# Optimization experiments

Hardware: AMD Instinct MI355X
Metric: run time of the kernel (lower is better)

## Reference

```python
import jax, jax.numpy as jnp
import numpy as np

B, S, H, D = 2, 2048, 16, 64


def setup_inputs() -> dict:
    key = jax.random.key(0)
    kq, kk, kv, km = jax.random.split(key, 4)
    q = jax.random.normal(kq, (B, S, H, D), dtype=jnp.float32)
    k = jax.random.normal(kk, (B, S, H, D), dtype=jnp.float32)
    v = jax.random.normal(kv, (B, S, H, D), dtype=jnp.float32)
    key_padding_mask = jax.random.randint(km, (B, S), 0, 2).astype(bool)
    return {"q": q, "k": k, "v": v, "key_padding_mask": key_padding_mask}


def reference(q, k, v, key_padding_mask):
    # [B,S,H,D] -> [B,H,S,D]; fp32 upcast (inputs already fp32)
    qt = jnp.transpose(q, (0, 2, 1, 3)).astype(jnp.float32)
    kt = jnp.transpose(k, (0, 2, 1, 3)).astype(jnp.float32)
    vt = jnp.transpose(v, (0, 2, 1, 3)).astype(jnp.float32)
    scale = D ** (-0.5)
    # [B,H,Sq,Sk]
    scores = jnp.einsum("bhqd,bhkd->bhqk", qt, kt) * scale
    # masked_fill where key_padding_mask is True -> -inf
    mask = key_padding_mask[:, None, None, :]  # [B,1,1,Sk]
    scores = jnp.where(mask, -jnp.inf, scores)
    attn = jax.nn.softmax(scores, axis=-1)
    out = jnp.einsum("bhqk,bhkd->bhqd", attn, vt).astype(q.dtype)
    # back to [B,S,H,D]
    return jnp.transpose(out, (0, 2, 1, 3))
```

## Files before the change

### kernel.cpp

```cpp
#include <hip/hip_runtime.h>
#include <hip/hip_bf16.h>

#define BB 2
#define SS 2048
#define HH 16
#define DD 64
#define BR 128
#define BC 64
#define NT (SS / BC)
#define NQT (SS / BR)
#define TILE_E (BC * DD)
#define TILE_B (TILE_E * 2)
#define LOG2E 1.44269504f
#define LSTR 72
#define OSZ (BB * SS * HH * DD)

typedef __attribute__((ext_vector_type(8))) short short8;
typedef __attribute__((ext_vector_type(4))) float f32x4;
typedef __attribute__((ext_vector_type(16))) float f32x16;
typedef __attribute__((ext_vector_type(4))) unsigned int uint32x4;
typedef __attribute__((ext_vector_type(4))) unsigned short ushort4_t;

static __device__ __forceinline__ unsigned short f2bf(float f) {
    unsigned int u = __float_as_uint(f);
    unsigned int r = u + 0x7FFFu + ((u >> 16) & 1u);
    return (unsigned short)(r >> 16);
}
static __device__ __forceinline__ unsigned int cvtpk(float lo, float hi) {
    unsigned int r;
    asm("v_cvt_pk_bf16_f32 %0, %1, %2" : "=v"(r) : "v"(lo), "v"(hi));
    return r;
}
static __device__ __forceinline__ void pl32swap(unsigned int &a, unsigned int &b) {
#if __has_builtin(__builtin_amdgcn_permlane32_swap)
    const auto r = __builtin_amdgcn_permlane32_swap((int)a, (int)b, false, false);
    a = (unsigned int)r[0];
    b = (unsigned int)r[1];
#else
    asm("v_permlane32_swap_b32 %0, %1" : "+v"(a), "+v"(b));
#endif
}
static __device__ __forceinline__ float fexp2(float x) {
#if __has_builtin(__builtin_amdgcn_exp2f)
    return __builtin_amdgcn_exp2f(x);
#else
    return exp2f(x);
#endif
}
static __device__ __forceinline__ void gl_lds16(const void* g, void* l) {
    __builtin_amdgcn_global_load_lds(
        (const __attribute__((address_space(1))) void*)g,
        (__attribute__((address_space(3))) void*)l, 16, 0, 0);
}

__global__ __launch_bounds__(256, 2)
void prep_kernel(const float* __restrict__ K, const float* __restrict__ V,
                 const int* __restrict__ M,
                 unsigned short* __restrict__ Kb, unsigned short* __restrict__ Vt,
                 int* __restrict__ mcnt)
{
    __shared__ unsigned short Vl[DD * LSTR];

    const int t  = blockIdx.x & (NT - 1);
    const int b  = blockIdx.x >> 9;
    const int bh = blockIdx.x >> 5;
    const int tid = threadIdx.x;
    const size_t tile = (size_t)blockIdx.x * TILE_E;
    const size_t rs = (size_t)HH * DD;
    const float* kb0 = K + (((size_t)b * SS + t * BC) * HH + (bh & 15)) * DD;
    const float* vb0 = V + (((size_t)b * SS + t * BC) * HH + (bh & 15)) * DD;
    const int* mrow = M + (size_t)b * SS + t * BC;

    {
        const int p  = tid & 7;
        const int r0 = tid >> 3;
        #pragma unroll
        for (int half = 0; half < 2; ++half) {
            const int r = r0 + half * 32;
            const int c = p ^ (r & 7);
            const float sel = mrow[r] ? 0.0f : 1.0f;
            const float* ks = kb0 + (size_t)r * rs + c * 8;
            const float4 f0 = *(const float4*)ks;
            const float4 f1 = *(const float4*)(ks + 4);
            uint32x4 u;
            u[0] = cvtpk(f0.x * sel, f0.y * sel);
            u[1] = cvtpk(f0.z * sel, f0.w * sel);
            u[2] = cvtpk(f1.x * sel, f1.y * sel);
            u[3] = cvtpk(f1.z * sel, f1.w * sel);
            *(uint32x4*)(Kb + tile + r * 64 + p * 8) = u;
        }
    }
    {
        const int vr = tid >> 2;
        const int vc = tid & 3;
        const float sel = mrow[vr] ? 0.0f : 1.0f;
        const float* vp = vb0 + (size_t)vr * rs + vc * 16;
        #pragma unroll
        for (int i = 0; i < 4; ++i) {
            const float4 f = *(const float4*)(vp + i * 4);
            const int d = vc * 16 + i * 4;
            Vl[(d + 0) * LSTR + vr] = f2bf(f.x * sel);
            Vl[(d + 1) * LSTR + vr] = f2bf(f.y * sel);
            Vl[(d + 2) * LSTR + vr] = f2bf(f.z * sel);
            Vl[(d + 3) * LSTR + vr] = f2bf(f.w * sel);
        }
    }
    __syncthreads();
    {
        const int p  = tid & 7;
        const int r0 = tid >> 3;
        #pragma unroll
        for (int half = 0; half < 2; ++half) {
            const int r = r0 + half * 32;
            const int c = p ^ (r & 7);
            const short8 o = *(const short8*)&Vl[r * LSTR + c * 8];
            *(short8*)(Vt + tile + r * 64 + p * 8) = o;
        }
    }
    if ((bh & 15) == 0 && tid < 64) {
        const unsigned long long bal = __ballot(mrow[tid] != 0);
        if (tid == 0) mcnt[b * NT + t] = (int)__popcll(bal);
    }
}

template<bool SPLIT>
__global__ __launch_bounds__(256, 2)
void fa3_kernel(const float* __restrict__ Q,
                const unsigned short* __restrict__ Kb,
                const unsigned short* __restrict__ Vt,
                const int* __restrict__ mcnt,
                float* __restrict__ Op,
                float* __restrict__ Lp)
{
    __shared__ __align__(16) unsigned short Ks[2][2 * TILE_E];
    __shared__ __align__(16) unsigned short Vs[2][2 * TILE_E];

    const int nwg  = (SPLIT ? 2 * BB * HH * NQT : BB * HH * NQT);
    const int cpx  = nwg >> 3;
    const int blk  = (blockIdx.x & 7) * cpx + (blockIdx.x >> 3);

    const int qt  = blk & (NQT - 1);
    const int bh  = (blk >> 4) & 31;
    const int spl = SPLIT ? (blk >> 9) : 0;
    const int b   = bh >> 4;
    const int h   = bh & 15;
    const int kt0 = SPLIT ? spl * (NT / 2) : 0;
    const int ktn = SPLIT ? (NT / 2) : NT;

    const int tid  = threadIdx.x;
    const int wave = tid >> 6;
    const int lane = tid & 63;
    const int ln   = lane & 31;
    const int l5   = lane >> 5;

    const float qscale = 0.125f * LOG2E;
    const int qrow = qt * BR + wave * 32 + ln;
    const float* qp = Q + (((size_t)b * SS + qrow) * HH + h) * DD;
    short8 qf[4];
    #pragma unroll
    for (int t = 0; t < 4; ++t) {
        const int d0 = t * 16 + l5 * 8;
        const float4 f0 = *(const float4*)(qp + d0);
        const float4 f1 = *(const float4*)(qp + d0 + 4);
        uint32x4 u;
        u[0] = cvtpk(f0.x * qscale, f0.y * qscale);
        u[1] = cvtpk(f0.z * qscale, f0.w * qscale);
        u[2] = cvtpk(f1.x * qscale, f1.y * qscale);
        u[3] = cvtpk(f1.z * qscale, f1.w * qscale);
        qf[t] = __builtin_bit_cast(short8, u);
    }

    int corr = 0;
    for (int i = 0; i < ktn; ++i) corr += mcnt[b * NT + kt0 + i];

    f32x16 acc0, acc1;
    #pragma unroll
    for (int i = 0; i < 16; ++i) { acc0[i] = 0.f; acc1[i] = 0.f; }
    f32x4 lsum4 = {0.f, 0.f, 0.f, 0.f};

    const unsigned short* kb_bh = Kb + (size_t)bh * NT * TILE_E;
    const unsigned short* vt_bh = Vt + (size_t)bh * NT * TILE_E;
    const int we = wave * 1024;
    const int wb = wave * 2048;

    {
        const unsigned short* kbt = kb_bh + (size_t)kt0 * TILE_E;
        const unsigned short* vtt = vt_bh + (size_t)kt0 * TILE_E;
        #pragma unroll
        for (int s = 0; s < 2; ++s) {
            gl_lds16(kbt + s * TILE_E + we + lane * 8,       (char*)Ks[0] + s * TILE_B + wb);
            gl_lds16(kbt + s * TILE_E + we + 512 + lane * 8, (char*)Ks[0] + s * TILE_B + wb + 1024);
            gl_lds16(vtt + s * TILE_E + we + lane * 8,       (char*)Vs[0] + s * TILE_B + wb);
            gl_lds16(vtt + s * TILE_E + we + 512 + lane * 8, (char*)Vs[0] + s * TILE_B + wb + 1024);
        }
    }
    __syncthreads();

    const int pswz = (ln & 7);
    const int npair = ktn >> 1;

    for (int ii = 0; ii < npair; ++ii) {
        const int cur = ii & 1;
        const int nxt = cur ^ 1;
        const int kn = kt0 + 2 * ((ii + 1 < npair) ? ii + 1 : ii);
        const unsigned short* kbt = kb_bh + (size_t)kn * TILE_E;
        const unsigned short* vtt = vt_bh + (size_t)kn * TILE_E;
        #pragma unroll
        for (int s = 0; s < 2; ++s) {
            gl_lds16(kbt + s * TILE_E + we + lane * 8,       (char*)Ks[nxt] + s * TILE_B + wb);
            gl_lds16(kbt + s * TILE_E + we + 512 + lane * 8, (char*)Ks[nxt] + s * TILE_B + wb + 1024);
            gl_lds16(vtt + s * TILE_E + we + lane * 8,       (char*)Vs[nxt] + s * TILE_B + wb);
            gl_lds16(vtt + s * TILE_E + we + 512 + lane * 8, (char*)Vs[nxt] + s * TILE_B + wb + 1024);
        }

        #pragma unroll
        for (int sub = 0; sub < 2; ++sub) {
            const unsigned short* Kt = Ks[cur] + sub * TILE_E;
            const unsigned short* Vtl = Vs[cur] + sub * TILE_E;

            f32x16 s0, s1;
            #pragma unroll
            for (int i = 0; i < 16; ++i) { s0[i] = 0.f; s1[i] = 0.f; }
            #pragma unroll
            for (int t = 0; t < 4; ++t) {
                const int p = (2 * t + l5) ^ pswz;
                const short8 kf0 = *(const short8*)(Kt + ln * 64 + p * 8);
                const short8 kf1 = *(const short8*)(Kt + (32 + ln) * 64 + p * 8);
                s0 = __builtin_amdgcn_mfma_f32_32x32x16_bf16(kf0, qf[t], s0, 0, 0, 0);
                s1 = __builtin_amdgcn_mfma_f32_32x32x16_bf16(kf1, qf[t], s1, 0, 0, 0);
            }

            unsigned int pk[2][8];
            #pragma unroll
            for (int hh = 0; hh < 2; ++hh) {
                #pragma unroll
                for (int g = 0; g < 4; ++g) {
                    const float p0 = fexp2(hh ? s1[g * 4 + 0] : s0[g * 4 + 0]);
                    const float p1 = fexp2(hh ? s1[g * 4 + 1] : s0[g * 4 + 1]);
                    const float p2 = fexp2(hh ? s1[g * 4 + 2] : s0[g * 4 + 2]);
                    const float p3 = fexp2(hh ? s1[g * 4 + 3] : s0[g * 4 + 3]);
                    lsum4 += (f32x4){p0, p1, p2, p3};
                    pk[hh][g * 2 + 0] = cvtpk(p0, p1);
                    pk[hh][g * 2 + 1] = cvtpk(p2, p3);
                }
            }
            #pragma unroll
            for (int hh = 0; hh < 2; ++hh) {
                pl32swap(pk[hh][0], pk[hh][2]);
                pl32swap(pk[hh][1], pk[hh][3]);
                pl32swap(pk[hh][4], pk[hh][6]);
                pl32swap(pk[hh][5], pk[hh][7]);
            }
            short8 pf[4];
            #pragma unroll
            for (int t = 0; t < 4; ++t) {
                const int hh = t >> 1;
                const int s4 = (t & 1) * 4;
                uint32x4 u;
                u[0] = pk[hh][s4 + 0];
                u[1] = pk[hh][s4 + 1];
                u[2] = pk[hh][s4 + 2];
                u[3] = pk[hh][s4 + 3];
                pf[t] = __builtin_bit_cast(short8, u);
            }

            #pragma unroll
            for (int t = 0; t < 4; ++t) {
                const int p = (2 * t + l5) ^ pswz;
                const short8 vf0 = *(const short8*)(Vtl + ln * 64 + p * 8);
                const short8 vf1 = *(const short8*)(Vtl + (32 + ln) * 64 + p * 8);
                acc0 = __builtin_amdgcn_mfma_f32_32x32x16_bf16(vf0, pf[t], acc0, 0, 0, 0);
                acc1 = __builtin_amdgcn_mfma_f32_32x32x16_bf16(vf1, pf[t], acc1, 0, 0, 0);
            }
        }

        __syncthreads();
    }

    const float lsum = (lsum4[0] + lsum4[1]) + (lsum4[2] + lsum4[3]);
    const float l = lsum + __shfl_xor(lsum, 32) - (float)corr;
    if (SPLIT) {
        float* op = Op + (size_t)spl * OSZ + (((size_t)b * SS + qrow) * HH + h) * DD;
        #pragma unroll
        for (int dh = 0; dh < 2; ++dh) {
            #pragma unroll
            for (int g = 0; g < 4; ++g) {
                const int d0 = dh * 32 + 8 * g + 4 * l5;
                float4 o;
                o.x = dh ? acc1[g * 4 + 0] : acc0[g * 4 + 0];
                o.y = dh ? acc1[g * 4 + 1] : acc0[g * 4 + 1];
                o.z = dh ? acc1[g * 4 + 2] : acc0[g * 4 + 2];
                o.w = dh ? acc1[g * 4 + 3] : acc0[g * 4 + 3];
                *(float4*)(op + d0) = o;
            }
        }
        if (l5 == 0)
            Lp[spl * (BB * HH * SS) + (b * HH + h) * SS + qrow] = l;
    } else {
        const float inv = 1.0f / l;
        float* op = Op + (((size_t)b * SS + qrow) * HH + h) * DD;
        #pragma unroll
        for (int dh = 0; dh < 2; ++dh) {
            #pragma unroll
            for (int g = 0; g < 4; ++g) {
                const int d0 = dh * 32 + 8 * g + 4 * l5;
                float4 o;
                o.x = (dh ? acc1[g * 4 + 0] : acc0[g * 4 + 0]) * inv;
                o.y = (dh ? acc1[g * 4 + 1] : acc0[g * 4 + 1]) * inv;
                o.z = (dh ? acc1[g * 4 + 2] : acc0[g * 4 + 2]) * inv;
                o.w = (dh ? acc1[g * 4 + 3] : acc0[g * 4 + 3]) * inv;
                *(float4*)(op + d0) = o;
            }
        }
    }
}

#define KP 72
#define FBR 64
__global__ __launch_bounds__(256, 2)
void fa_fallback(const float* __restrict__ Q, const float* __restrict__ K,
                 const float* __restrict__ V, const int* __restrict__ M,
                 float* __restrict__ O)
{
    __shared__ unsigned short KsF[BC][KP];
    __shared__ unsigned short VsF[DD][KP];
    __shared__ unsigned short PsF[4][16][KP];
    __shared__ float mb[BC];

    const int blk = blockIdx.x;
    const int qt = blk % (SS / FBR);
    const int bh = blk / (SS / FBR);
    const int b = bh / HH;
    const int h = bh % HH;
    const int tid = threadIdx.x;
    const int wave = tid >> 6;
    const int lane = tid & 63;
    const int lq = lane & 15;
    const int quad = lane >> 4;

    const int qrow = qt * FBR + wave * 16 + lq;
    const float* qp = Q + (((size_t)b * SS + qrow) * HH + h) * DD;
    short8 qf[2];
    #pragma unroll
    for (int c = 0; c < 2; ++c) {
        const float4 f0 = *(const float4*)(qp + c * 32 + quad * 8);
        const float4 f1 = *(const float4*)(qp + c * 32 + quad * 8 + 4);
        short8 t;
        t[0] = (short)f2bf(f0.x * 0.125f); t[1] = (short)f2bf(f0.y * 0.125f);
        t[2] = (short)f2bf(f0.z * 0.125f); t[3] = (short)f2bf(f0.w * 0.125f);
        t[4] = (short)f2bf(f1.x * 0.125f); t[5] = (short)f2bf(f1.y * 0.125f);
        t[6] = (short)f2bf(f1.z * 0.125f); t[7] = (short)f2bf(f1.w * 0.125f);
        qf[c] = t;
    }
    f32x4 acc[4];
    #pragma unroll
    for (int dt = 0; dt < 4; ++dt) acc[dt] = (f32x4){0.f, 0.f, 0.f, 0.f};
    float m_i[4] = {-1e30f, -1e30f, -1e30f, -1e30f};
    float l_i[4] = {0.f, 0.f, 0.f, 0.f};

    const int sr = tid >> 2;
    const int sc = tid & 3;
    const size_t rowstride = (size_t)HH * DD;
    const float* kbase = K + (((size_t)b * SS) * HH + h) * DD;
    const float* vbase = V + (((size_t)b * SS) * HH + h) * DD;

    for (int kt = 0; kt < NT; ++kt) {
        const int k0 = kt * BC;
        __syncthreads();
        {
            const float* kp = kbase + (size_t)(k0 + sr) * rowstride + sc * 16;
            #pragma unroll
            for (int i = 0; i < 4; ++i) {
                const float4 f = *(const float4*)(kp + i * 4);
                ushort4_t u;
                u[0] = f2bf(f.x); u[1] = f2bf(f.y); u[2] = f2bf(f.z); u[3] = f2bf(f.w);
                *(ushort4_t*)&KsF[sr][sc * 16 + i * 4] = u;
            }
            const float* vp = vbase + (size_t)(k0 + sr) * rowstride + sc * 16;
            #pragma unroll
            for (int i = 0; i < 4; ++i) {
                const float4 f = *(const float4*)(vp + i * 4);
                const int d = sc * 16 + i * 4;
                VsF[d + 0][sr] = f2bf(f.x); VsF[d + 1][sr] = f2bf(f.y);
                VsF[d + 2][sr] = f2bf(f.z); VsF[d + 3][sr] = f2bf(f.w);
            }
            if (tid < BC) mb[tid] = M[(size_t)b * SS + k0 + tid] ? -1e30f : 0.0f;
        }
        __syncthreads();
        f32x4 s[4];
        #pragma unroll
        for (int ct = 0; ct < 4; ++ct) {
            f32x4 z = (f32x4){0.f, 0.f, 0.f, 0.f};
            const unsigned short* kr = &KsF[ct * 16 + lq][quad * 8];
            const short8 kf0 = *(const short8*)kr;
            const short8 kf1 = *(const short8*)(kr + 32);
            z = __builtin_amdgcn_mfma_f32_16x16x32_bf16(qf[0], kf0, z, 0, 0, 0);
            z = __builtin_amdgcn_mfma_f32_16x16x32_bf16(qf[1], kf1, z, 0, 0, 0);
            s[ct] = z;
        }
        #pragma unroll
        for (int ct = 0; ct < 4; ++ct) {
            const float mbias = mb[ct * 16 + lq];
            s[ct][0] += mbias; s[ct][1] += mbias; s[ct][2] += mbias; s[ct][3] += mbias;
        }
        #pragma unroll
        for (int r = 0; r < 4; ++r) {
            float mx = fmaxf(fmaxf(s[0][r], s[1][r]), fmaxf(s[2][r], s[3][r]));
            mx = fmaxf(mx, __shfl_xor(mx, 1));
            mx = fmaxf(mx, __shfl_xor(mx, 2));
            mx = fmaxf(mx, __shfl_xor(mx, 4));
            mx = fmaxf(mx, __shfl_xor(mx, 8));
            const float m_new = fmaxf(m_i[r], mx);
            const float alpha = __expf(m_i[r] - m_new);
            m_i[r] = m_new;
            float rs = 0.f;
            #pragma unroll
            for (int ct = 0; ct < 4; ++ct) {
                const float p = __expf(s[ct][r] - m_new);
                rs += p;
                PsF[wave][quad * 4 + r][ct * 16 + lq] = f2bf(p);
            }
            rs += __shfl_xor(rs, 1); rs += __shfl_xor(rs, 2);
            rs += __shfl_xor(rs, 4); rs += __shfl_xor(rs, 8);
            l_i[r] = l_i[r] * alpha + rs;
            #pragma unroll
            for (int dt = 0; dt < 4; ++dt) acc[dt][r] *= alpha;
        }
        const unsigned short* pr = &PsF[wave][lq][quad * 8];
        const short8 pf0 = *(const short8*)pr;
        const short8 pf1 = *(const short8*)(pr + 32);
        #pragma unroll
        for (int dt = 0; dt < 4; ++dt) {
            const unsigned short* vr = &VsF[dt * 16 + lq][quad * 8];
            const short8 vf0 = *(const short8*)vr;
            const short8 vf1 = *(const short8*)(vr + 32);
            acc[dt] = __builtin_amdgcn_mfma_f32_16x16x32_bf16(pf0, vf0, acc[dt], 0, 0, 0);
            acc[dt] = __builtin_amdgcn_mfma_f32_16x16x32_bf16(pf1, vf1, acc[dt], 0, 0, 0);
        }
    }
    #pragma unroll
    for (int r = 0; r < 4; ++r) {
        const float inv = 1.0f / l_i[r];
        const int row = qt * FBR + wave * 16 + quad * 4 + r;
        float* op = O + (((size_t)b * SS + row) * HH + h) * DD;
        #pragma unroll
        for (int dt = 0; dt < 4; ++dt)
            op[dt * 16 + lq] = acc[dt][r] * inv;
    }
}

extern "C" void kernel_launch(void* const* d_in, const int* in_sizes, int n_in,
                              void* d_out, int out_size, void* d_ws, size_t ws_size,
                              hipStream_t stream) {
    const float* q = (const float*)d_in[0];
    const float* k = (const float*)d_in[1];
    const float* v = (const float*)d_in[2];
    const int*   m = (const int*)d_in[3];
    float* out = (float*)d_out;

    const int nprep = BB * HH * NT;
    const size_t kb_bytes = (size_t)nprep * TILE_E * 2;
    const size_t mc_bytes = (size_t)BB * NT * 4;
    const size_t need_single = 2 * kb_bytes + mc_bytes;

    if (ws_size >= need_single) {
        unsigned short* Kb = (unsigned short*)d_ws;
        unsigned short* Vt = (unsigned short*)((char*)d_ws + kb_bytes);
        int* mcnt = (int*)((char*)d_ws + 2 * kb_bytes);
        prep_kernel<<<nprep, 256, 0, stream>>>(k, v, m, Kb, Vt, mcnt);
        fa3_kernel<false><<<BB * HH * NQT, 256, 0, stream>>>(
            q, Kb, Vt, mcnt, out, nullptr);
    } else {
        fa_fallback<<<BB * HH * (SS / FBR), 256, 0, stream>>>(q, k, v, m, out);
    }
}
```

Measured before the change: 134.2 us.

## Batch QK and PV MFMAs across both key subtiles and raise wave priority

Restructures the inner loop so all QK^T MFMAs for both 64-key subtiles are issued together, then both exponentials and packings, then all PV MFMAs, rather than alternating per subtile. MFMA bursts are wrapped in s_setprio so waves in matrix phases get issue priority while other waves do exp work. The goal is longer independent MFMA chains and better overlap of matrix and vector work between waves. It raises register pressure (four score accumulators plus two P fragment sets), which may lower occupancy.

```diff
diff --git a/kernel.cpp b/kernel.cpp
--- a/kernel.cpp
+++ b/kernel.cpp
@@ -213,32 +213,53 @@
             gl_lds16(vtt + s * TILE_E + we + 512 + lane * 8, (char*)Vs[nxt] + s * TILE_B + wb + 1024);
         }
 
+        const unsigned short* Kt0 = Ks[cur];
+        const unsigned short* Kt1 = Ks[cur] + TILE_E;
+        const unsigned short* Vt0 = Vs[cur];
+        const unsigned short* Vt1 = Vs[cur] + TILE_E;
+
+        f32x16 s00, s01, s10, s11;
+        #pragma unroll
+        for (int i = 0; i < 16; ++i) { s00[i] = 0.f; s01[i] = 0.f; s10[i] = 0.f; s11[i] = 0.f; }
+        __builtin_amdgcn_s_setprio(1);
+        #pragma unroll
+        for (int t = 0; t < 4; ++t) {
+            const int p = (2 * t + l5) ^ pswz;
+            const short8 kA0 = *(const short8*)(Kt0 + ln * 64 + p * 8);
+            const short8 kA1 = *(const short8*)(Kt0 + (32 + ln) * 64 + p * 8);
+            const short8 kB0 = *(const short8*)(Kt1 + ln * 64 + p * 8);
+            const short8 kB1 = *(const short8*)(Kt1 + (32 + ln) * 64 + p * 8);
+            s00 = __builtin_amdgcn_mfma_f32_32x32x16_bf16(kA0, qf[t], s00, 0, 0, 0);
+            s01 = __builtin_amdgcn_mfma_f32_32x32x16_bf16(kA1, qf[t], s01, 0, 0, 0);
+            s10 = __builtin_amdgcn_mfma_f32_32x32x16_bf16(kB0, qf[t], s10, 0, 0, 0);
+            s11 = __builtin_amdgcn_mfma_f32_32x32x16_bf16(kB1, qf[t], s11, 0, 0, 0);
+        }
+        __builtin_amdgcn_s_setprio(0);
+
+        short8 pfa[4], pfb[4];
         #pragma unroll
         for (int sub = 0; sub < 2; ++sub) {
-            const unsigned short* Kt = Ks[cur] + sub * TILE_E;
-            const unsigned short* Vtl = Vs[cur] + sub * TILE_E;
-
-            f32x16 s0, s1;
-            #pragma unroll
-            for (int i = 0; i < 16; ++i) { s0[i] = 0.f; s1[i] = 0.f; }
-            #pragma unroll
-            for (int t = 0; t < 4; ++t) {
-                const int p = (2 * t + l5) ^ pswz;
-                const short8 kf0 = *(const short8*)(Kt + ln * 64 + p * 8);
-                const short8 kf1 = *(const short8*)(Kt + (32 + ln) * 64 + p * 8);
-                s0 = __builtin_amdgcn_mfma_f32_32x32x16_bf16(kf0, qf[t], s0, 0, 0, 0);
-                s1 = __builtin_amdgcn_mfma_f32_32x32x16_bf16(kf1, qf[t], s1, 0, 0, 0);
-            }
-
             unsigned int pk[2][8];
             #pragma unroll
             for (int hh = 0; hh < 2; ++hh) {
                 #pragma unroll
                 for (int g = 0; g < 4; ++g) {
-                    const float p0 = fexp2(hh ? s1[g * 4 + 0] : s0[g * 4 + 0]);
-                    const float p1 = fexp2(hh ? s1[g * 4 + 1] : s0[g * 4 + 1]);
-                    const float p2 = fexp2(hh ? s1[g * 4 + 2] : s0[g * 4 + 2]);
-                    const float p3 = fexp2(hh ? s1[g * 4 + 3] : s0[g * 4 + 3]);
+                    float e0, e1, e2, e3;
+                    if (sub == 0) {
+                        e0 = hh ? s01[g * 4 + 0] : s00[g * 4 + 0];
+                        e1 = hh ? s01[g * 4 + 1] : s00[g * 4 + 1];
+                        e2 = hh ? s01[g * 4 + 2] : s00[g * 4 + 2];
+                        e3 = hh ? s01[g * 4 + 3] : s00[g * 4 + 3];
+                    } else {
+                        e0 = hh ? s11[g * 4 + 0] : s10[g * 4 + 0];
+                        e1 = hh ? s11[g * 4 + 1] : s10[g * 4 + 1];
+                        e2 = hh ? s11[g * 4 + 2] : s10[g * 4 + 2];
+                        e3 = hh ? s11[g * 4 + 3] : s10[g * 4 + 3];
+                    }
+                    const float p0 = fexp2(e0);
+                    const float p1 = fexp2(e1);
+                    const float p2 = fexp2(e2);
+                    const float p3 = fexp2(e3);
                     lsum4 += (f32x4){p0, p1, p2, p3};
                     pk[hh][g * 2 + 0] = cvtpk(p0, p1);
                     pk[hh][g * 2 + 1] = cvtpk(p2, p3);
@@ -251,7 +272,6 @@
                 pl32swap(pk[hh][4], pk[hh][6]);
                 pl32swap(pk[hh][5], pk[hh][7]);
             }
-            short8 pf[4];
             #pragma unroll
             for (int t = 0; t < 4; ++t) {
                 const int hh = t >> 1;
@@ -261,18 +281,29 @@
                 u[1] = pk[hh][s4 + 1];
                 u[2] = pk[hh][s4 + 2];
                 u[3] = pk[hh][s4 + 3];
-                pf[t] = __builtin_bit_cast(short8, u);
-            }
-
-            #pragma unroll
-            for (int t = 0; t < 4; ++t) {
-                const int p = (2 * t + l5) ^ pswz;
-                const short8 vf0 = *(const short8*)(Vtl + ln * 64 + p * 8);
-                const short8 vf1 = *(const short8*)(Vtl + (32 + ln) * 64 + p * 8);
-                acc0 = __builtin_amdgcn_mfma_f32_32x32x16_bf16(vf0, pf[t], acc0, 0, 0, 0);
-                acc1 = __builtin_amdgcn_mfma_f32_32x32x16_bf16(vf1, pf[t], acc1, 0, 0, 0);
-            }
-        }
+                if (sub == 0) pfa[t] = __builtin_bit_cast(short8, u);
+                else          pfb[t] = __builtin_bit_cast(short8, u);
+            }
+        }
+
+        __builtin_amdgcn_s_setprio(1);
+        #pragma unroll
+        for (int t = 0; t < 4; ++t) {
+            const int p = (2 * t + l5) ^ pswz;
+            const short8 vf0 = *(const short8*)(Vt0 + ln * 64 + p * 8);
+            const short8 vf1 = *(const short8*)(Vt0 + (32 + ln) * 64 + p * 8);
+            acc0 = __builtin_amdgcn_mfma_f32_32x32x16_bf16(vf0, pfa[t], acc0, 0, 0, 0);
+            acc1 = __builtin_amdgcn_mfma_f32_32x32x16_bf16(vf1, pfa[t], acc1, 0, 0, 0);
+        }
+        #pragma unroll
+        for (int t = 0; t < 4; ++t) {
+            const int p = (2 * t + l5) ^ pswz;
+            const short8 vf0 = *(const short8*)(Vt1 + ln * 64 + p * 8);
+            const short8 vf1 = *(const short8*)(Vt1 + (32 + ln) * 64 + p * 8);
+            acc0 = __builtin_amdgcn_mfma_f32_32x32x16_bf16(vf0, pfb[t], acc0, 0, 0, 0);
+            acc1 = __builtin_amdgcn_mfma_f32_32x32x16_bf16(vf1, pfb[t], acc1, 0, 0, 0);
+        }
+        __builtin_amdgcn_s_setprio(0);
 
         __syncthreads();
     }
```

Result: slower. 137.1 us (+2.1%).
